# Performance work log

Hardware: AMD Instinct MI355X
Metric: run time of the kernel (lower is better)

Reference implementation:

```python
import jax, jax.numpy as jnp
import numpy as np

B, T, V, D = 128, 128, 64, 32
Q, E, PLM = 5, 8, 768
D_STATIC, N_CLASS = 16, 2
ALPHA = 0.5


def _glorot(key, shape):
    lim = (6.0 / (shape[-2] + shape[-1])) ** 0.5
    return jax.random.uniform(key, shape, jnp.float32, -lim, lim)


def setup_inputs() -> dict:
    key = jax.random.key(0)
    ks = jax.random.split(key, 30)
    data = jax.random.normal(ks[0], (B, T, V), jnp.float32)
    mask = (jax.random.uniform(ks[1], (B, T, V)) < 0.3).astype(jnp.float32)
    P = jnp.concatenate([data, mask], axis=-1)  # [b, t, 2v]
    return {
        "P": P,
        "P_static": jax.random.normal(ks[2], (B, D_STATIC), jnp.float32),
        "P_avg_interval": jax.random.uniform(ks[3], (B, T, V)) * 10.0,
        "P_length": jax.random.randint(ks[4], (B, 1), T // 2, T + 1),
        "P_time": jax.random.uniform(ks[5], (B, T)),
        "P_var_plm_rep_tensor": jax.random.normal(ks[6], (V, PLM), jnp.float32),
        # Value_Encoder: Linear(1, D) + ReLU
        "w_val": _glorot(ks[7], (1, D))[0], "b_val": jnp.zeros((D,), jnp.float32),
        # Time_Encoder: periodic Linear(1, D-1), linear Linear(1, 1)
        "w_per": _glorot(ks[8], (1, D - 1))[0], "b_per": jnp.zeros((D - 1,), jnp.float32),
        "w_lin": _glorot(ks[9], (1, 1))[0], "b_lin": jnp.zeros((1,), jnp.float32),
        "emb1": jax.random.normal(ks[10], (V, D), jnp.float32),
        # prior_to_state MLP: PLM -> 2D -> Q
        "Ws1": _glorot(ks[11], (PLM, 2 * D)), "bs1": jnp.zeros((2 * D,), jnp.float32),
        "Ws2": _glorot(ks[12], (2 * D, Q)), "bs2": jnp.zeros((Q,), jnp.float32),
        # prior_to_graph MLP: PLM -> 2D -> E
        "Wg1": _glorot(ks[13], (PLM, 2 * D)), "bg1": jnp.zeros((2 * D,), jnp.float32),
        "Wg2": _glorot(ks[14], (2 * D, E)), "bg2": jnp.zeros((E,), jnp.float32),
        "rarity_W": jax.random.normal(ks[15], (V, V), jnp.float32),
        # hypernet gate params (nodes_num == Q): W [Q, 2D+1, D], b [Q, D]
        "Wu": _glorot(ks[16], (Q, 2 * D + 1, D)), "bu": _glorot(ks[17], (Q, D)),
        "Wr": _glorot(ks[18], (Q, 2 * D + 1, D)), "br": _glorot(ks[19], (Q, D)),
        "Wcand": _glorot(ks[20], (Q, 2 * D + 1, D)), "bcand": _glorot(ks[21], (Q, D)),
        # static embedding + classifier
        "W_se": _glorot(ks[22], (D_STATIC, V)), "b_se": jnp.zeros((V,), jnp.float32),
        "Wc1": _glorot(ks[23], (2 * V, 200)), "bc1": jnp.zeros((200,), jnp.float32),
        "Wc2": _glorot(ks[24], (200, N_CLASS)), "bc2": jnp.zeros((N_CLASS,), jnp.float32),
    }


def _forward(P, P_static, P_avg_interval, P_length, P_time, P_var_plm_rep_tensor,
             w_val, b_val, w_per, b_per, w_lin, b_lin, emb1,
             Ws1, bs1, Ws2, bs2, Wg1, bg1, Wg2, bg2, rarity_W,
             Wu, bu, Wr, br, Wcand, bcand, W_se, b_se, Wc1, bc1, Wc2, bc2):
    b, t, v2 = P.shape
    v = v2 // 2
    d = emb1.shape[1]
    data, mask = P[:, :, :v], P[:, :, v:]            # [b,t,v] each
    mk = mask[..., None]
    # embeddings: value + absolute time + node embedding, all masked
    value_emb = jax.nn.relu(data[..., None] * w_val + b_val) * mk          # [b,t,v,d]
    tt = P_time[:, :, None, None]                                          # [b,t,1,1]
    time_emb = jnp.concatenate([tt * w_lin + b_lin,
                                jnp.sin(tt * w_per + b_per)], -1) * mk     # [b,t,v,d]
    obs_emb = (value_emb + time_emb + emb1[None, None]) * mk               # [b,t,v,d]

    # PLM-prior hypernet vectors (identical across batch -> computed once, broadcast)
    var_vector = jax.nn.relu(P_var_plm_rep_tensor @ Ws1 + bs1) @ Ws2 + bs2  # [v,Q]
    gvec = jax.nn.relu(P_var_plm_rep_tensor @ Wg1 + bg1) @ Wg2 + bg2        # [v,E]
    gvec = gvec / jnp.maximum(jnp.linalg.norm(gvec, axis=-1, keepdims=True), 1e-12)
    adj = jax.nn.softmax(gvec @ gvec.T, axis=-1)                            # [v,v]

    var_total_obs = mask.sum(axis=1)                                        # [b,v]
    eye = jnp.eye(v, dtype=P.dtype)
    lengths = P_length[:, 0].astype(jnp.int32)                              # [b]

    def gate(inp, W, bb):
        # hypernet-generated per-node GRU gate: einsum('nd,dio->nio') + bmm, fused
        return (jnp.einsum('bvi,vq,qio->bvo', inp, var_vector, W)
                + jnp.einsum('vq,qo->vo', var_vector, bb))

    def step(carry, xs):
        h, out = carry
        cur_obs, m, cur_avg, s = xs
        rarity = ALPHA * jnp.tanh(cur_avg / (var_total_obs + 1.0))          # [b,v]
        rsm = -rarity_W * jnp.abs(rarity[:, :, None] - rarity[:, None, :])  # [b,v,v]
        amask = m[:, :, None] * m[:, None, :]   # rows of unobserved zeroed, observed cols = 1
        cur_adj = adj * (1.0 + rsm) * amask * (1.0 - eye) + eye             # [b,v,v]
        x = jnp.concatenate([cur_obs, rarity[..., None]], -1)               # [b,v,d+1]
        comb = jnp.einsum('bij,bjk->bik', cur_adj, jnp.concatenate([x, h], -1))
        r = jax.nn.sigmoid(gate(comb, Wr, br))
        u = jax.nn.sigmoid(gate(comb, Wu, bu))
        h_r = r * h  # original mutates h[nodes_ind] = r*h[nodes_ind] before candidate
        cand = jnp.tanh(gate(jnp.concatenate([x, h_r], -1), Wcand, bcand))
        h_new = (1.0 - u) * h_r + u * cand
        h = jnp.where((m > 0.5)[..., None], h_new, h)  # scatter only observed nodes
        out = jnp.where((s == lengths - 1)[:, None, None], h, out)
        return (h, out), None

    xs = (jnp.moveaxis(obs_emb, 1, 0), jnp.moveaxis(mask, 1, 0),
          jnp.moveaxis(P_avg_interval, 1, 0), jnp.arange(t, dtype=jnp.int32))
    h0 = jnp.zeros((b, v, d), P.dtype)
    (_, output), _ = jax.lax.scan(step, (h0, jnp.zeros_like(h0)), xs)

    static_emb = P_static @ W_se + b_se                                     # [b,v]
    feat = jnp.concatenate([output.sum(-1), static_emb], -1)                # [b,2v]
    return jax.nn.relu(feat @ Wc1 + bc1) @ Wc2 + bc2                        # [b,n_class]


def reference(P, P_static, P_avg_interval, P_length, P_time, P_var_plm_rep_tensor,
              w_val, b_val, w_per, b_per, w_lin, b_lin, emb1,
              Ws1, bs1, Ws2, bs2, Wg1, bg1, Wg2, bg2, rarity_W,
              Wu, bu, Wr, br, Wcand, bcand, W_se, b_se, Wc1, bc1, Wc2, bc2):
    return _forward(P, P_static, P_avg_interval, P_length, P_time, P_var_plm_rep_tensor,
                    w_val, b_val, w_per, b_per, w_lin, b_lin, emb1,
                    Ws1, bs1, Ws2, bs2, Wg1, bg1, Wg2, bg2, rarity_W,
                    Wu, bu, Wr, br, Wcand, bcand, W_se, b_se, Wc1, bc1, Wc2, bc2)
```

## Files before the change

kernel.cpp:

```cpp
#include <hip/hip_runtime.h>
#include <hip/hip_bf16.h>
#include <math.h>

#define BB 128
#define TT 128
#define VV 64
#define DD 32
#define NQ 5

typedef short bf16x8 __attribute__((ext_vector_type(8)));
typedef float f32x4 __attribute__((ext_vector_type(4)));

#define MFMA(a,b,c) __builtin_amdgcn_mfma_f32_16x16x32_bf16(a,b,c,0,0,0)

__device__ __forceinline__ float sigm(float x){ return 1.0f/(1.0f+__expf(-x)); }
__device__ __forceinline__ float tanhfast(float x){ return 2.0f/(1.0f+__expf(-2.0f*x)) - 1.0f; }
__device__ __forceinline__ unsigned short f2bf(float x){
  unsigned u = __float_as_uint(x);
  u += 0x7FFFu + ((u>>16)&1u);
  return (unsigned short)(u>>16);
}
__device__ __forceinline__ float bf2f(unsigned short h){
  return __uint_as_float(((unsigned)h)<<16);
}

union bfu { bf16x8 v; unsigned u[4]; unsigned short s[8]; };

__device__ __forceinline__ void split8(const float* x, bfu& H, bfu& L){
  #pragma unroll
  for (int i = 0; i < 4; ++i){
    const float a = x[2*i], c = x[2*i+1];
    const __hip_bfloat162 hp = __float22bfloat162_rn(make_float2(a, c));
    unsigned hu; __builtin_memcpy(&hu, &hp, 4);
    H.u[i] = hu;
    const float ah = __uint_as_float(hu << 16);
    const float ch = __uint_as_float(hu & 0xFFFF0000u);
    const __hip_bfloat162 lp = __float22bfloat162_rn(make_float2(a - ah, c - ch));
    unsigned lu; __builtin_memcpy(&lu, &lp, 4);
    L.u[i] = lu;
  }
}

__device__ __forceinline__ void split4(const float* x, unsigned* H, unsigned* L){
  #pragma unroll
  for (int i = 0; i < 2; ++i){
    const float a = x[2*i], c = x[2*i+1];
    const __hip_bfloat162 hp = __float22bfloat162_rn(make_float2(a, c));
    unsigned hu; __builtin_memcpy(&hu, &hp, 4);
    H[i] = hu;
    const float ah = __uint_as_float(hu << 16);
    const float ch = __uint_as_float(hu & 0xFFFF0000u);
    const __hip_bfloat162 lp = __float22bfloat162_rn(make_float2(a - ah, c - ch));
    unsigned lu; __builtin_memcpy(&lu, &lp, 4);
    L[i] = lu;
  }
}


__global__ __launch_bounds__(64)
void k_mlp(const float* __restrict__ Pplm,
           const float* __restrict__ Ws1, const float* __restrict__ bs1,
           const float* __restrict__ Ws2, const float* __restrict__ bs2,
           const float* __restrict__ Wg1, const float* __restrict__ bg1,
           const float* __restrict__ Wg2, const float* __restrict__ bg2,
           float* __restrict__ vv_ws, float* __restrict__ gn_ws)
{
  __shared__ float sH[64], sG[64], sgv[8];
  const int v = blockIdx.x, j = threadIdx.x;
  float a = bs1[j], g = bg1[j];
  for (int k = 0; k < 768; ++k){
    const float p = Pplm[v*768 + k];
    a = fmaf(p, Ws1[k*64 + j], a);
    g = fmaf(p, Wg1[k*64 + j], g);
  }
  sH[j] = fmaxf(a, 0.f);
  sG[j] = fmaxf(g, 0.f);
  __syncthreads();
  if (j < 5){
    float acc = bs2[j];
    for (int k = 0; k < 64; ++k) acc = fmaf(sH[k], Ws2[k*5 + j], acc);
    vv_ws[v*5 + j] = acc;
  }
  if (j < 8){
    float acc = bg2[j];
    for (int k = 0; k < 64; ++k) acc = fmaf(sG[k], Wg2[k*8 + j], acc);
    sgv[j] = acc;
  }
  __syncthreads();
  if (j == 0){
    float n = 0.f;
    for (int e = 0; e < 8; ++e) n += sgv[e]*sgv[e];
    n = fmaxf(sqrtf(n), 1e-12f);
    for (int e = 0; e < 8; ++e) gn_ws[v*8 + e] = sgv[e]/n;
  }
}

__global__ __launch_bounds__(64)
void k_adj(const float* __restrict__ gn_ws, float* __restrict__ adj_ws)
{
  const int v = blockIdx.x, j = threadIdx.x;
  float sc = 0.f;
  #pragma unroll
  for (int e = 0; e < 8; ++e) sc += gn_ws[v*8+e]*gn_ws[j*8+e];
  float mx = sc;
  for (int off = 32; off > 0; off >>= 1) mx = fmaxf(mx, __shfl_xor(mx, off));
  const float ex = __expf(sc - mx);
  float sm = ex;
  for (int off = 32; off > 0; off >>= 1) sm += __shfl_xor(sm, off);
  adj_ws[v*64 + j] = ex / sm;
}

__global__ __launch_bounds__(256)
void k_vto(const float* __restrict__ P, float* __restrict__ vto_ws)
{
  const int idx = blockIdx.x*256 + threadIdx.x;
  if (idx >= BB*VV) return;
  const int b = idx/VV, v = idx%VV;
  float s = 0.f;
  for (int t = 0; t < TT; ++t) s += P[((size_t)(b*TT+t))*128 + 64 + v];
  vto_ws[idx] = s;
}

__global__ __launch_bounds__(256)
void k_bpack(const float* __restrict__ Wr, const float* __restrict__ br,
             const float* __restrict__ Wu, const float* __restrict__ bu,
             const float* __restrict__ Wc, const float* __restrict__ bc,
             unsigned short* __restrict__ Bru, unsigned short* __restrict__ Bcn,
             float* __restrict__ sideRU, float* __restrict__ sideC)
{
  const int idx = blockIdx.x*256 + threadIdx.x;
  if (idx < 20480){
    const int f = idx >> 9, rem = idx & 511, l = rem >> 3, j = rem & 7;
    const int p = f & 1, kt = (f>>1)&1, e = f>>2;
    const int kp = kt*32 + (l>>4)*8 + j;
    const int k = (kp < 32) ? kp : kp + 1;
    const int o = p*16 + (l&15);
    const int q = (e < 5) ? e : e - 5;
    const float* W = (e < 5) ? Wr : Wu;
    Bru[idx] = f2bf(W[(q*65 + k)*32 + o]);
  } else if (idx < 30720){
    const int i2 = idx - 20480;
    const int f = i2 >> 9, rem = i2 & 511, l = rem >> 3, j = rem & 7;
    const int p = f & 1, kt = (f>>1)&1, e = f>>2;
    const int kp = kt*32 + (l>>4)*8 + j;
    const int k = (kp < 32) ? kp : kp + 1;
    const int o = p*16 + (l&15);
    Bcn[i2] = f2bf(Wc[(e*65 + k)*32 + o]);
  } else if (idx < 31360){
    const int i3 = idx - 30720;
    const int e = i3 >> 6, rem = i3 & 63, o = rem >> 1, s = rem & 1;
    const int q = (e < 5) ? e : e - 5;
    float v;
    if (s == 0) v = (e < 5) ? Wr[(q*65 + 32)*32 + o] : Wu[(q*65 + 32)*32 + o];
    else        v = (e < 5) ? br[q*32 + o] : bu[q*32 + o];
    sideRU[i3] = v;
  } else if (idx < 31680){
    const int i4 = idx - 31360;
    const int e = i4 >> 6, rem = i4 & 63, o = rem >> 1, s = rem & 1;
    sideC[i4] = s ? bc[e*32 + o] : Wc[(e*65 + 32)*32 + o];
  }
}


__global__ __launch_bounds__(512, 1)
void tedgn_main(const float* __restrict__ P, const float* __restrict__ Pstatic,
                const float* __restrict__ Pavg, const int* __restrict__ Plen,
                const float* __restrict__ Ptime,
                const float* __restrict__ w_val, const float* __restrict__ b_val,
                const float* __restrict__ w_per, const float* __restrict__ b_per,
                const float* __restrict__ w_lin, const float* __restrict__ b_lin,
                const float* __restrict__ emb1, const float* __restrict__ rarW,
                const float* __restrict__ Wse, const float* __restrict__ bse,
                const float* __restrict__ Wc1, const float* __restrict__ bc1,
                const float* __restrict__ Wc2, const float* __restrict__ bc2,
                const float* __restrict__ vv_ws, const float* __restrict__ adjb_ws,
                const float* __restrict__ vto_ws,
                const unsigned short* __restrict__ Bru_ws,
                const unsigned short* __restrict__ Bc_ws,
                const float* __restrict__ sideRU_ws, const float* __restrict__ sideC_ws,
                float* __restrict__ out)
{
  __shared__ __align__(16) unsigned short B0T[2][2][64][72];
  __shared__ __align__(16) unsigned short s_Wru[20480];
  __shared__ __align__(16) unsigned short s_Wc[10240];
  __shared__ __align__(16) float A1f[4][16][68];
  __shared__ __align__(16) float hrF[4][16][36];
  __shared__ __align__(16) float s_rar[2][64];
  __shared__ __align__(16) float s_m[2][64];
  __shared__ float s_sru[640], s_scd[320];
  __shared__ float s_outf[64][33];
  __shared__ float s_feat[128], s_hid[200];

  const int tid  = threadIdx.x;
  const int lane = tid & 63;
  const int wid  = tid >> 6;
  const int mq   = wid >> 1;
  const int ph   = wid & 1;
  const int l15  = lane & 15;
  const int l16g = lane >> 4;
  const int kgo  = l16g * 8;
  const int R    = mq * 16;
  const int v_own = R + l15;
  const int oo   = ph*16 + l15;
  const int b    = blockIdx.x;
  const int len  = Plen[b];

  for (int i = tid; i < 640; i += 512) s_sru[i] = sideRU_ws[i];
  for (int i = tid; i < 320; i += 512) s_scd[i] = sideC_ws[i];
  {
    const uint4* src1 = (const uint4*)Bru_ws;
    uint4* dst1 = (uint4*)s_Wru;
    for (int i = tid; i < 2560; i += 512) dst1[i] = src1[i];
    const uint4* src2 = (const uint4*)Bc_ws;
    uint4* dst2 = (uint4*)s_Wc;
    for (int i = tid; i < 1280; i += 512) dst2[i] = src2[i];
  }

  float adjb_r[2][8], rarW_r[2][8];
  #pragma unroll
  for (int kt = 0; kt < 2; ++kt)
    #pragma unroll
    for (int j = 0; j < 8; ++j){
      adjb_r[kt][j] = adjb_ws[v_own*64 + kt*32 + kgo + j];
      rarW_r[kt][j] = rarW   [v_own*64 + kt*32 + kgo + j];
    }
  float embr[8], wvr[8], bvr[8], wpr[8], bpr[8];
  #pragma unroll
  for (int j = 0; j < 8; ++j){
    const int d = kgo + j;
    embr[j] = emb1[v_own*DD + d];
    wvr[j]  = w_val[d];
    bvr[j]  = b_val[d];
    wpr[j]  = (d == 0) ? w_lin[0] : w_per[d-1];
    bpr[j]  = (d == 0) ? b_lin[0] : b_per[d-1];
  }
  float vvr[4][NQ];
  #pragma unroll
  for (int j = 0; j < 4; ++j)
    #pragma unroll
    for (int q = 0; q < NQ; ++q)
      vvr[j][q] = vv_ws[(R + l16g*4 + j)*NQ + q];
  const float vto_own = vto_ws[b*VV + v_own];

  float h[4]    = {0.f,0.f,0.f,0.f};
  float outr[4] = {0.f,0.f,0.f,0.f};
  bfu xfH, xfL;
  float rar_own, m_own;

  {
    const float pd = P[(size_t)(b*TT)*128 + v_own];
    const float pm = P[(size_t)(b*TT)*128 + 64 + v_own];
    const float pa = Pavg[(size_t)(b*TT)*VV + v_own];
    const float pt = Ptime[b*TT];
    const float rar_n = 0.5f * tanhfast(pa / (vto_own + 1.f));
    float xv[8];
    #pragma unroll
    for (int j = 0; j < 8; ++j){
      const int d = kgo + j;
      const float tearg = fmaf(pt, wpr[j], bpr[j]);
      const float te = (d == 0) ? tearg : __sinf(tearg);
      const float ve = fmaxf(fmaf(pd, wvr[j], bvr[j]), 0.f);
      xv[j] = (ve + te + embr[j]) * pm;
    }
    split8(xv, xfH, xfL);
    if (ph == 0){
      #pragma unroll
      for (int j = 0; j < 8; ++j){
        B0T[0][0][kgo + j][v_own] = xfH.s[j];
        B0T[0][1][kgo + j][v_own] = xfL.s[j];
      }
      *(uint2*)&B0T[0][0][32 + l15][R + l16g*4] = make_uint2(0u, 0u);
      *(uint2*)&B0T[0][1][32 + l15][R + l16g*4] = make_uint2(0u, 0u);
      if (l16g == 0){
        s_rar[0][v_own] = rar_n;
        s_m[0][v_own]   = pm;
      }
    } else {
      *(uint2*)&B0T[0][0][48 + l15][R + l16g*4] = make_uint2(0u, 0u);
      *(uint2*)&B0T[0][1][48 + l15][R + l16g*4] = make_uint2(0u, 0u);
    }
    rar_own = rar_n;
    m_own   = pm;
  }
  __syncthreads();

  #pragma clang loop unroll(disable)
  for (int t = 0; t < TT; ++t){
    const int cur = t & 1, nxt = cur ^ 1;

    float pd = 0.f, pm = 0.f, pa = 0.f, pt = 0.f;
    const bool more = (t + 1 < TT);
    if (more){
      pd = P[(size_t)(b*TT + t + 1)*128 + v_own];
      pm = P[(size_t)(b*TT + t + 1)*128 + 64 + v_own];
      pa = Pavg[(size_t)(b*TT + t + 1)*VV + v_own];
      pt = Ptime[b*TT + t + 1];
    }

    {
      bfu aAh[2], aAl[2];
      float crar = 0.f;
      #pragma unroll
      for (int kt = 0; kt < 2; ++kt){
        const float4 r0 = *(const float4*)&s_rar[cur][kt*32 + kgo];
        const float4 r1 = *(const float4*)&s_rar[cur][kt*32 + kgo + 4];
        const float4 m0 = *(const float4*)&s_m[cur][kt*32 + kgo];
        const float4 m1 = *(const float4*)&s_m[cur][kt*32 + kgo + 4];
        const float rj[8] = {r0.x,r0.y,r0.z,r0.w,r1.x,r1.y,r1.z,r1.w};
        const float mj[8] = {m0.x,m0.y,m0.z,m0.w,m1.x,m1.y,m1.z,m1.w};
        float av[8];
        #pragma unroll
        for (int j = 0; j < 8; ++j){
          const int k = kt*32 + kgo + j;
          const float e1 = fmaf(-rarW_r[kt][j], fabsf(rar_own - rj[j]), 1.0f);
          const float a  = adjb_r[kt][j] * e1 * (m_own * mj[j]);
          av[j] = (k == v_own) ? 1.0f : a;
          crar = fmaf(av[j], rj[j], crar);
        }
        split8(av, aAh[kt], aAl[kt]);
      }
      crar += __shfl_xor(crar, 16);
      crar += __shfl_xor(crar, 32);
      if (ph == 0 && l16g == 0) A1f[mq][l15][64] = crar;

      #pragma unroll
      for (int ni = 0; ni < 2; ++ni){
        const int n = 2*ph + ni;
        f32x4 acc = {0.f,0.f,0.f,0.f};
        #pragma unroll
        for (int kt = 0; kt < 2; ++kt){
          const bf16x8 bh = *(const bf16x8*)&B0T[cur][0][n*16 + l15][kt*32 + kgo];
          const bf16x8 bl = *(const bf16x8*)&B0T[cur][1][n*16 + l15][kt*32 + kgo];
          acc = MFMA(aAh[kt].v, bh, acc);
          acc = MFMA(aAl[kt].v, bh, acc);
          acc = MFMA(aAh[kt].v, bl, acc);
        }
        const int col = n*16 + l15;
        #pragma unroll
        for (int j = 0; j < 4; ++j) A1f[mq][l16g*4 + j][col] = acc[j];
      }
    }
    __syncthreads();

    float hr[4], uu[4];
    {
      bfu aH[2], aL[2];
      #pragma unroll
      for (int kt = 0; kt < 2; ++kt){
        float xv[8];
        *(float4*)&xv[0] = *(const float4*)&A1f[mq][l15][kt*32 + kgo];
        *(float4*)&xv[4] = *(const float4*)&A1f[mq][l15][kt*32 + kgo + 4];
        split8(xv, aH[kt], aL[kt]);
      }
      float a64f[4];
      #pragma unroll
      for (int j = 0; j < 4; ++j) a64f[j] = A1f[mq][l16g*4 + j][64];

      f32x4 ag[10];
      #pragma unroll
      for (int e = 0; e < 10; ++e){
        const float2 wb = *(const float2*)&s_sru[e*64 + oo*2];
        #pragma unroll
        for (int j = 0; j < 4; ++j) ag[e][j] = fmaf(a64f[j], wb.x, wb.y);
      }
      #pragma unroll
      for (int e = 0; e < 10; ++e){
        const bf16x8 w0 = *(const bf16x8*)&s_Wru[(((e*2+0)*2+ph)*64 + lane)*8];
        const bf16x8 w1 = *(const bf16x8*)&s_Wru[(((e*2+1)*2+ph)*64 + lane)*8];
        ag[e] = MFMA(aH[0].v, w0, ag[e]);
        ag[e] = MFMA(aL[0].v, w0, ag[e]);
        ag[e] = MFMA(aH[1].v, w1, ag[e]);
        ag[e] = MFMA(aL[1].v, w1, ag[e]);
      }
      #pragma unroll
      for (int j = 0; j < 4; ++j){
        const float pr = vvr[j][0]*ag[0][j] + vvr[j][1]*ag[1][j]
                       + vvr[j][2]*ag[2][j] + vvr[j][3]*ag[3][j]
                       + vvr[j][4]*ag[4][j];
        hr[j] = sigm(pr) * h[j];
        hrF[mq][l16g*4 + j][oo] = hr[j];
      }
      #pragma unroll
      for (int j = 0; j < 4; ++j){
        const float pu = vvr[j][0]*ag[5][j] + vvr[j][1]*ag[6][j]
                       + vvr[j][2]*ag[7][j] + vvr[j][3]*ag[8][j]
                       + vvr[j][4]*ag[9][j];
        uu[j] = sigm(pu);
      }
    }
    __syncthreads();

    {
      bfu hH, hL;
      {
        float hv[8];
        *(float4*)&hv[0] = *(const float4*)&hrF[mq][l15][kgo];
        *(float4*)&hv[4] = *(const float4*)&hrF[mq][l15][kgo + 4];
        split8(hv, hH, hL);
      }
      float rar_cj[4], m_cj[4];
      #pragma unroll
      for (int j = 0; j < 4; ++j){
        rar_cj[j] = s_rar[cur][R + l16g*4 + j];
        m_cj[j]   = s_m[cur][R + l16g*4 + j];
      }
      f32x4 ag[5];
      #pragma unroll
      for (int e = 0; e < 5; ++e){
        const float2 wb = *(const float2*)&s_scd[e*64 + oo*2];
        #pragma unroll
        for (int j = 0; j < 4; ++j) ag[e][j] = fmaf(rar_cj[j], wb.x, wb.y);
      }
      #pragma unroll
      for (int e = 0; e < 5; ++e){
        const bf16x8 w0 = *(const bf16x8*)&s_Wc[(((e*2+0)*2+ph)*64 + lane)*8];
        const bf16x8 w1 = *(const bf16x8*)&s_Wc[(((e*2+1)*2+ph)*64 + lane)*8];
        ag[e] = MFMA(xfH.v, w0, ag[e]);
        ag[e] = MFMA(xfL.v, w0, ag[e]);
        ag[e] = MFMA(hH.v,  w1, ag[e]);
        ag[e] = MFMA(hL.v,  w1, ag[e]);
      }
      const bool snap = (t == len - 1);
      #pragma unroll
      for (int j = 0; j < 4; ++j){
        const float pc = vvr[j][0]*ag[0][j] + vvr[j][1]*ag[1][j]
                       + vvr[j][2]*ag[2][j] + vvr[j][3]*ag[3][j]
                       + vvr[j][4]*ag[4][j];
        const float cd = tanhfast(pc);
        const float hn = fmaf(uu[j], cd - hr[j], hr[j]);
        const float hf = (m_cj[j] > 0.5f) ? hn : h[j];
        h[j] = hf;
        if (snap) outr[j] = hf;
      }
      {
        unsigned H2[2], L2[2];
        split4(h, H2, L2);
        *(uint2*)&B0T[nxt][0][32 + oo][R + l16g*4] = make_uint2(H2[0], H2[1]);
        *(uint2*)&B0T[nxt][1][32 + oo][R + l16g*4] = make_uint2(L2[0], L2[1]);
      }
      if (more){
        const float rar_n = 0.5f * tanhfast(pa / (vto_own + 1.f));
        float xv[8];
        #pragma unroll
        for (int j = 0; j < 8; ++j){
          const int d = kgo + j;
          const float tearg = fmaf(pt, wpr[j], bpr[j]);
          const float te = (d == 0) ? tearg : __sinf(tearg);
          const float ve = fmaxf(fmaf(pd, wvr[j], bvr[j]), 0.f);
          xv[j] = (ve + te + embr[j]) * pm;
        }
        split8(xv, xfH, xfL);
        if (ph == 0){
          #pragma unroll
          for (int j = 0; j < 8; ++j){
            B0T[nxt][0][kgo + j][v_own] = xfH.s[j];
            B0T[nxt][1][kgo + j][v_own] = xfL.s[j];
          }
          if (l16g == 0){
            s_rar[nxt][v_own] = rar_n;
            s_m[nxt][v_own]   = pm;
          }
        }
        rar_own = rar_n;
        m_own   = pm;
      }
    }
    __syncthreads();
  }

  #pragma unroll
  for (int j = 0; j < 4; ++j)
    s_outf[R + l16g*4 + j][oo] = outr[j];
  __syncthreads();
  if (tid < VV){
    float s = 0.f;
    #pragma unroll
    for (int d = 0; d < DD; ++d) s += s_outf[tid][d];
    s_feat[tid] = s;
  } else if (tid < 2*VV){
    const int v = tid - VV;
    float se = bse[v];
    #pragma unroll
    for (int k = 0; k < 16; ++k) se = fmaf(Pstatic[b*16 + k], Wse[k*VV + v], se);
    s_feat[VV + v] = se;
  }
  __syncthreads();
  if (tid < 200){
    float a = bc1[tid];
    for (int k = 0; k < 128; ++k) a = fmaf(s_feat[k], Wc1[k*200 + tid], a);
    s_hid[tid] = fmaxf(a, 0.f);
  }
  __syncthreads();
  if (tid < 2){
    float a = bc2[tid];
    for (int k = 0; k < 200; ++k) a = fmaf(s_hid[k], Wc2[k*2 + tid], a);
    out[b*2 + tid] = a;
  }
}


extern "C" void kernel_launch(void* const* d_in, const int* in_sizes, int n_in,
                              void* d_out, int out_size, void* d_ws, size_t ws_size,
                              hipStream_t stream) {
  (void)in_sizes; (void)n_in; (void)out_size; (void)ws_size;
  const float* P       = (const float*)d_in[0];
  const float* Pstatic = (const float*)d_in[1];
  const float* Pavg    = (const float*)d_in[2];
  const int*   Plen    = (const int*)  d_in[3];
  const float* Ptime   = (const float*)d_in[4];
  const float* Pplm    = (const float*)d_in[5];
  const float* w_val   = (const float*)d_in[6];
  const float* b_val   = (const float*)d_in[7];
  const float* w_per   = (const float*)d_in[8];
  const float* b_per   = (const float*)d_in[9];
  const float* w_lin   = (const float*)d_in[10];
  const float* b_lin   = (const float*)d_in[11];
  const float* emb1    = (const float*)d_in[12];
  const float* Ws1     = (const float*)d_in[13];
  const float* bs1     = (const float*)d_in[14];
  const float* Ws2     = (const float*)d_in[15];
  const float* bs2     = (const float*)d_in[16];
  const float* Wg1     = (const float*)d_in[17];
  const float* bg1     = (const float*)d_in[18];
  const float* Wg2     = (const float*)d_in[19];
  const float* bg2     = (const float*)d_in[20];
  const float* rarW    = (const float*)d_in[21];
  const float* Wu      = (const float*)d_in[22];
  const float* bu      = (const float*)d_in[23];
  const float* Wr      = (const float*)d_in[24];
  const float* br      = (const float*)d_in[25];
  const float* Wcand   = (const float*)d_in[26];
  const float* bcand   = (const float*)d_in[27];
  const float* Wse     = (const float*)d_in[28];
  const float* bse     = (const float*)d_in[29];
  const float* Wc1     = (const float*)d_in[30];
  const float* bc1     = (const float*)d_in[31];
  const float* Wc2     = (const float*)d_in[32];
  const float* bc2     = (const float*)d_in[33];

  float* ws = (float*)d_ws;
  float*          vv_ws   = ws;
  float*          gn_ws   = ws + 320;
  float*          adjb_ws = ws + 832;
  float*          vto_ws  = ws + 4928;
  unsigned short* Bru_ws  = (unsigned short*)(ws + 13120);
  unsigned short* Bc_ws   = (unsigned short*)(ws + 23360);
  float*          sideRU_ws = ws + 28480;
  float*          sideC_ws  = ws + 29120;

  k_mlp  <<<64, 64, 0, stream>>>(Pplm, Ws1, bs1, Ws2, bs2, Wg1, bg1, Wg2, bg2, vv_ws, gn_ws);
  k_adj  <<<64, 64, 0, stream>>>(gn_ws, adjb_ws);
  k_vto  <<<(BB*VV + 255)/256, 256, 0, stream>>>(P, vto_ws);
  k_bpack<<<124, 256, 0, stream>>>(Wr, br, Wu, bu, Wcand, bcand, Bru_ws, Bc_ws, sideRU_ws, sideC_ws);

  tedgn_main<<<BB, 512, 0, stream>>>(P, Pstatic, Pavg, Plen, Ptime,
                                     w_val, b_val, w_per, b_per, w_lin, b_lin,
                                     emb1, rarW, Wse, bse, Wc1, bc1, Wc2, bc2,
                                     vv_ws, adjb_ws, vto_ws,
                                     Bru_ws, Bc_ws, sideRU_ws, sideC_ws,
                                     (float*)d_out);
}
```

Measured before the change: 586.2 us.

## Transpose MFMA operand roles to drop A1f staging and one barrier per step

Swaps the A/B operand roles in the graph-aggregation and gate MFMAs, so each lane ends up holding the rows its own node needs. The aggregated features then feed the gate MFMAs straight from registers instead of going through the A1f shared buffer and an extra __syncthreads each timestep. The packed weight layouts in k_bpack are permuted to match the new fragment order. The next-step input embedding is computed earlier to overlap with the MFMAs, and per-node state becomes scalars instead of 4-row arrays. In exchange, the h writeback now uses scalar scattered shared stores, which may add bank conflicts.

Measured after the change: 639.3 us. 9.1% more time.

```diff
diff --git a/kernel.cpp b/kernel.cpp
--- a/kernel.cpp
+++ b/kernel.cpp
@@ -38,21 +38,6 @@
     const __hip_bfloat162 lp = __float22bfloat162_rn(make_float2(a - ah, c - ch));
     unsigned lu; __builtin_memcpy(&lu, &lp, 4);
     L.u[i] = lu;
-  }
-}
-
-__device__ __forceinline__ void split4(const float* x, unsigned* H, unsigned* L){
-  #pragma unroll
-  for (int i = 0; i < 2; ++i){
-    const float a = x[2*i], c = x[2*i+1];
-    const __hip_bfloat162 hp = __float22bfloat162_rn(make_float2(a, c));
-    unsigned hu; __builtin_memcpy(&hu, &hp, 4);
-    H[i] = hu;
-    const float ah = __uint_as_float(hu << 16);
-    const float ch = __uint_as_float(hu & 0xFFFF0000u);
-    const __hip_bfloat162 lp = __float22bfloat162_rn(make_float2(a - ah, c - ch));
-    unsigned lu; __builtin_memcpy(&lu, &lp, 4);
-    L[i] = lu;
   }
 }
 
@@ -131,20 +116,21 @@
   const int idx = blockIdx.x*256 + threadIdx.x;
   if (idx < 20480){
     const int f = idx >> 9, rem = idx & 511, l = rem >> 3, j = rem & 7;
-    const int p = f & 1, kt = (f>>1)&1, e = f>>2;
-    const int kp = kt*32 + (l>>4)*8 + j;
-    const int k = (kp < 32) ? kp : kp + 1;
-    const int o = p*16 + (l&15);
+    const int ph = f & 1, kt = (f>>1)&1, e = f>>2;
+    const int l15 = l & 15, l16g = l >> 4;
+    const int fslot = (kt*2 + (j>>2))*16 + l16g*4 + (j&3);
+    const int k = (fslot < 32) ? fslot : fslot + 1;
+    const int o = ph*16 + l15;
     const int q = (e < 5) ? e : e - 5;
     const float* W = (e < 5) ? Wr : Wu;
     Bru[idx] = f2bf(W[(q*65 + k)*32 + o]);
   } else if (idx < 30720){
     const int i2 = idx - 20480;
     const int f = i2 >> 9, rem = i2 & 511, l = rem >> 3, j = rem & 7;
-    const int p = f & 1, kt = (f>>1)&1, e = f>>2;
-    const int kp = kt*32 + (l>>4)*8 + j;
-    const int k = (kp < 32) ? kp : kp + 1;
-    const int o = p*16 + (l&15);
+    const int ph = f & 1, kt = (f>>1)&1, e = f>>2;
+    const int l15 = l & 15, l16g = l >> 4;
+    const int k = (kt == 0) ? (l16g*8 + j) : (33 + l16g*8 + j);
+    const int o = ph*16 + l15;
     Bcn[i2] = f2bf(Wc[(e*65 + k)*32 + o]);
   } else if (idx < 31360){
     const int i3 = idx - 30720;
@@ -183,7 +169,6 @@
   __shared__ __align__(16) unsigned short B0T[2][2][64][72];
   __shared__ __align__(16) unsigned short s_Wru[20480];
   __shared__ __align__(16) unsigned short s_Wc[10240];
-  __shared__ __align__(16) float A1f[4][16][68];
   __shared__ __align__(16) float hrF[4][16][36];
   __shared__ __align__(16) float s_rar[2][64];
   __shared__ __align__(16) float s_m[2][64];
@@ -201,7 +186,7 @@
   const int kgo  = l16g * 8;
   const int R    = mq * 16;
   const int v_own = R + l15;
-  const int oo   = ph*16 + l15;
+  const int ob   = ph*16 + l16g*4;
   const int b    = blockIdx.x;
   const int len  = Plen[b];
 
@@ -234,17 +219,14 @@
     wpr[j]  = (d == 0) ? w_lin[0] : w_per[d-1];
     bpr[j]  = (d == 0) ? b_lin[0] : b_per[d-1];
   }
-  float vvr[4][NQ];
+  float vv_own[NQ];
   #pragma unroll
-  for (int j = 0; j < 4; ++j)
-    #pragma unroll
-    for (int q = 0; q < NQ; ++q)
-      vvr[j][q] = vv_ws[(R + l16g*4 + j)*NQ + q];
+  for (int q = 0; q < NQ; ++q) vv_own[q] = vv_ws[v_own*NQ + q];
   const float vto_own = vto_ws[b*VV + v_own];
 
   float h[4]    = {0.f,0.f,0.f,0.f};
   float outr[4] = {0.f,0.f,0.f,0.f};
-  bfu xfH, xfL;
+  bfu xfH, xfL, xfnH, xfnL;
   float rar_own, m_own;
 
   {
@@ -287,6 +269,7 @@
   #pragma clang loop unroll(disable)
   for (int t = 0; t < TT; ++t){
     const int cur = t & 1, nxt = cur ^ 1;
+    const float rar_cur = rar_own, m_cur = m_own;
 
     float pd = 0.f, pm = 0.f, pa = 0.f, pt = 0.f;
     const bool more = (t + 1 < TT);
@@ -297,95 +280,118 @@
       pt = Ptime[b*TT + t + 1];
     }
 
-    {
-      bfu aAh[2], aAl[2];
-      float crar = 0.f;
+    bfu aAh[2], aAl[2];
+    float crar = 0.f;
+    #pragma unroll
+    for (int kt = 0; kt < 2; ++kt){
+      const float4 r0 = *(const float4*)&s_rar[cur][kt*32 + kgo];
+      const float4 r1 = *(const float4*)&s_rar[cur][kt*32 + kgo + 4];
+      const float4 m0 = *(const float4*)&s_m[cur][kt*32 + kgo];
+      const float4 m1 = *(const float4*)&s_m[cur][kt*32 + kgo + 4];
+      const float rj[8] = {r0.x,r0.y,r0.z,r0.w,r1.x,r1.y,r1.z,r1.w};
+      const float mj[8] = {m0.x,m0.y,m0.z,m0.w,m1.x,m1.y,m1.z,m1.w};
+      float av[8];
+      #pragma unroll
+      for (int j = 0; j < 8; ++j){
+        const int k = kt*32 + kgo + j;
+        const float e1 = fmaf(-rarW_r[kt][j], fabsf(rar_cur - rj[j]), 1.0f);
+        const float a  = adjb_r[kt][j] * e1 * (m_cur * mj[j]);
+        av[j] = (k == v_own) ? 1.0f : a;
+        crar = fmaf(av[j], rj[j], crar);
+      }
+      split8(av, aAh[kt], aAl[kt]);
+    }
+    crar += __shfl_xor(crar, 16);
+    crar += __shfl_xor(crar, 32);
+
+    f32x4 Dv[4];
+    #pragma unroll
+    for (int ft = 0; ft < 4; ++ft){
+      f32x4 acc = {0.f,0.f,0.f,0.f};
       #pragma unroll
       for (int kt = 0; kt < 2; ++kt){
-        const float4 r0 = *(const float4*)&s_rar[cur][kt*32 + kgo];
-        const float4 r1 = *(const float4*)&s_rar[cur][kt*32 + kgo + 4];
-        const float4 m0 = *(const float4*)&s_m[cur][kt*32 + kgo];
-        const float4 m1 = *(const float4*)&s_m[cur][kt*32 + kgo + 4];
-        const float rj[8] = {r0.x,r0.y,r0.z,r0.w,r1.x,r1.y,r1.z,r1.w};
-        const float mj[8] = {m0.x,m0.y,m0.z,m0.w,m1.x,m1.y,m1.z,m1.w};
-        float av[8];
+        const bf16x8 ah = *(const bf16x8*)&B0T[cur][0][ft*16 + l15][kt*32 + kgo];
+        const bf16x8 al = *(const bf16x8*)&B0T[cur][1][ft*16 + l15][kt*32 + kgo];
+        acc = MFMA(ah, aAh[kt].v, acc);
+        acc = MFMA(al, aAh[kt].v, acc);
+        acc = MFMA(ah, aAl[kt].v, acc);
+      }
+      Dv[ft] = acc;
+    }
+
+    if (more){
+      const float rar_n = 0.5f * tanhfast(pa / (vto_own + 1.f));
+      float xv[8];
+      #pragma unroll
+      for (int j = 0; j < 8; ++j){
+        const int d = kgo + j;
+        const float tearg = fmaf(pt, wpr[j], bpr[j]);
+        const float te = (d == 0) ? tearg : __sinf(tearg);
+        const float ve = fmaxf(fmaf(pd, wvr[j], bvr[j]), 0.f);
+        xv[j] = (ve + te + embr[j]) * pm;
+      }
+      split8(xv, xfnH, xfnL);
+      if (ph == 0){
         #pragma unroll
         for (int j = 0; j < 8; ++j){
-          const int k = kt*32 + kgo + j;
-          const float e1 = fmaf(-rarW_r[kt][j], fabsf(rar_own - rj[j]), 1.0f);
-          const float a  = adjb_r[kt][j] * e1 * (m_own * mj[j]);
-          av[j] = (k == v_own) ? 1.0f : a;
-          crar = fmaf(av[j], rj[j], crar);
+          B0T[nxt][0][kgo + j][v_own] = xfnH.s[j];
+          B0T[nxt][1][kgo + j][v_own] = xfnL.s[j];
         }
-        split8(av, aAh[kt], aAl[kt]);
-      }
-      crar += __shfl_xor(crar, 16);
-      crar += __shfl_xor(crar, 32);
-      if (ph == 0 && l16g == 0) A1f[mq][l15][64] = crar;
-
-      #pragma unroll
-      for (int ni = 0; ni < 2; ++ni){
-        const int n = 2*ph + ni;
-        f32x4 acc = {0.f,0.f,0.f,0.f};
+        if (l16g == 0){
+          s_rar[nxt][v_own] = rar_n;
+          s_m[nxt][v_own]   = pm;
+        }
+      }
+      rar_own = rar_n;
+      m_own   = pm;
+    }
+
+    bfu cfH[2], cfL[2];
+    #pragma unroll
+    for (int kt = 0; kt < 2; ++kt){
+      float f8[8];
+      #pragma unroll
+      for (int j = 0; j < 8; ++j) f8[j] = Dv[kt*2 + (j>>2)][j&3];
+      split8(f8, cfH[kt], cfL[kt]);
+    }
+
+    float hr[4], uu[4];
+    {
+      f32x4 ag[10];
+      #pragma unroll
+      for (int e = 0; e < 10; ++e){
+        const float4 sp0 = *(const float4*)&s_sru[e*64 + ob*2];
+        const float4 sp1 = *(const float4*)&s_sru[e*64 + ob*2 + 4];
+        ag[e][0] = fmaf(crar, sp0.x, sp0.y);
+        ag[e][1] = fmaf(crar, sp0.z, sp0.w);
+        ag[e][2] = fmaf(crar, sp1.x, sp1.y);
+        ag[e][3] = fmaf(crar, sp1.z, sp1.w);
+      }
+      #pragma unroll
+      for (int e = 0; e < 10; ++e){
         #pragma unroll
         for (int kt = 0; kt < 2; ++kt){
-          const bf16x8 bh = *(const bf16x8*)&B0T[cur][0][n*16 + l15][kt*32 + kgo];
-          const bf16x8 bl = *(const bf16x8*)&B0T[cur][1][n*16 + l15][kt*32 + kgo];
-          acc = MFMA(aAh[kt].v, bh, acc);
-          acc = MFMA(aAl[kt].v, bh, acc);
-          acc = MFMA(aAh[kt].v, bl, acc);
+          const bf16x8 w = *(const bf16x8*)&s_Wru[(((e*2+kt)*2+ph)*64 + lane)*8];
+          ag[e] = MFMA(w, cfH[kt].v, ag[e]);
+          ag[e] = MFMA(w, cfL[kt].v, ag[e]);
         }
-        const int col = n*16 + l15;
-        #pragma unroll
-        for (int j = 0; j < 4; ++j) A1f[mq][l16g*4 + j][col] = acc[j];
-      }
-    }
-    __syncthreads();
-
-    float hr[4], uu[4];
-    {
-      bfu aH[2], aL[2];
-      #pragma unroll
-      for (int kt = 0; kt < 2; ++kt){
-        float xv[8];
-        *(float4*)&xv[0] = *(const float4*)&A1f[mq][l15][kt*32 + kgo];
-        *(float4*)&xv[4] = *(const float4*)&A1f[mq][l15][kt*32 + kgo + 4];
-        split8(xv, aH[kt], aL[kt]);
-      }
-      float a64f[4];
-      #pragma unroll
-      for (int j = 0; j < 4; ++j) a64f[j] = A1f[mq][l16g*4 + j][64];
-
-      f32x4 ag[10];
-      #pragma unroll
-      for (int e = 0; e < 10; ++e){
-        const float2 wb = *(const float2*)&s_sru[e*64 + oo*2];
-        #pragma unroll
-        for (int j = 0; j < 4; ++j) ag[e][j] = fmaf(a64f[j], wb.x, wb.y);
-      }
-      #pragma unroll
-      for (int e = 0; e < 10; ++e){
-        const bf16x8 w0 = *(const bf16x8*)&s_Wru[(((e*2+0)*2+ph)*64 + lane)*8];
-        const bf16x8 w1 = *(const bf16x8*)&s_Wru[(((e*2+1)*2+ph)*64 + lane)*8];
-        ag[e] = MFMA(aH[0].v, w0, ag[e]);
-        ag[e] = MFMA(aL[0].v, w0, ag[e]);
-        ag[e] = MFMA(aH[1].v, w1, ag[e]);
-        ag[e] = MFMA(aL[1].v, w1, ag[e]);
-      }
-      #pragma unroll
-      for (int j = 0; j < 4; ++j){
-        const float pr = vvr[j][0]*ag[0][j] + vvr[j][1]*ag[1][j]
-                       + vvr[j][2]*ag[2][j] + vvr[j][3]*ag[3][j]
-                       + vvr[j][4]*ag[4][j];
-        hr[j] = sigm(pr) * h[j];
-        hrF[mq][l16g*4 + j][oo] = hr[j];
-      }
-      #pragma unroll
-      for (int j = 0; j < 4; ++j){
-        const float pu = vvr[j][0]*ag[5][j] + vvr[j][1]*ag[6][j]
-                       + vvr[j][2]*ag[7][j] + vvr[j][3]*ag[8][j]
-                       + vvr[j][4]*ag[9][j];
-        uu[j] = sigm(pu);
+      }
+      float hr4[4];
+      #pragma unroll
+      for (int jj = 0; jj < 4; ++jj){
+        const float pr = vv_own[0]*ag[0][jj] + vv_own[1]*ag[1][jj]
+                       + vv_own[2]*ag[2][jj] + vv_own[3]*ag[3][jj]
+                       + vv_own[4]*ag[4][jj];
+        hr[jj] = sigm(pr) * h[jj];
+        hr4[jj] = hr[jj];
+      }
+      *(float4*)&hrF[mq][l15][ob] = make_float4(hr4[0], hr4[1], hr4[2], hr4[3]);
+      #pragma unroll
+      for (int jj = 0; jj < 4; ++jj){
+        const float pu = vv_own[0]*ag[5][jj] + vv_own[1]*ag[6][jj]
+                       + vv_own[2]*ag[7][jj] + vv_own[3]*ag[8][jj]
+                       + vv_own[4]*ag[9][jj];
+        uu[jj] = sigm(pu);
       }
     }
     __syncthreads();
@@ -398,79 +404,51 @@
         *(float4*)&hv[4] = *(const float4*)&hrF[mq][l15][kgo + 4];
         split8(hv, hH, hL);
       }
-      float rar_cj[4], m_cj[4];
-      #pragma unroll
-      for (int j = 0; j < 4; ++j){
-        rar_cj[j] = s_rar[cur][R + l16g*4 + j];
-        m_cj[j]   = s_m[cur][R + l16g*4 + j];
-      }
       f32x4 ag[5];
       #pragma unroll
       for (int e = 0; e < 5; ++e){
-        const float2 wb = *(const float2*)&s_scd[e*64 + oo*2];
-        #pragma unroll
-        for (int j = 0; j < 4; ++j) ag[e][j] = fmaf(rar_cj[j], wb.x, wb.y);
+        const float4 sp0 = *(const float4*)&s_scd[e*64 + ob*2];
+        const float4 sp1 = *(const float4*)&s_scd[e*64 + ob*2 + 4];
+        ag[e][0] = fmaf(rar_cur, sp0.x, sp0.y);
+        ag[e][1] = fmaf(rar_cur, sp0.z, sp0.w);
+        ag[e][2] = fmaf(rar_cur, sp1.x, sp1.y);
+        ag[e][3] = fmaf(rar_cur, sp1.z, sp1.w);
       }
       #pragma unroll
       for (int e = 0; e < 5; ++e){
         const bf16x8 w0 = *(const bf16x8*)&s_Wc[(((e*2+0)*2+ph)*64 + lane)*8];
         const bf16x8 w1 = *(const bf16x8*)&s_Wc[(((e*2+1)*2+ph)*64 + lane)*8];
-        ag[e] = MFMA(xfH.v, w0, ag[e]);
-        ag[e] = MFMA(xfL.v, w0, ag[e]);
-        ag[e] = MFMA(hH.v,  w1, ag[e]);
-        ag[e] = MFMA(hL.v,  w1, ag[e]);
+        ag[e] = MFMA(w0, xfH.v, ag[e]);
+        ag[e] = MFMA(w0, xfL.v, ag[e]);
+        ag[e] = MFMA(w1, hH.v,  ag[e]);
+        ag[e] = MFMA(w1, hL.v,  ag[e]);
       }
       const bool snap = (t == len - 1);
       #pragma unroll
-      for (int j = 0; j < 4; ++j){
-        const float pc = vvr[j][0]*ag[0][j] + vvr[j][1]*ag[1][j]
-                       + vvr[j][2]*ag[2][j] + vvr[j][3]*ag[3][j]
-                       + vvr[j][4]*ag[4][j];
+      for (int jj = 0; jj < 4; ++jj){
+        const float pc = vv_own[0]*ag[0][jj] + vv_own[1]*ag[1][jj]
+                       + vv_own[2]*ag[2][jj] + vv_own[3]*ag[3][jj]
+                       + vv_own[4]*ag[4][jj];
         const float cd = tanhfast(pc);
-        const float hn = fmaf(uu[j], cd - hr[j], hr[j]);
-        const float hf = (m_cj[j] > 0.5f) ? hn : h[j];
-        h[j] = hf;
-        if (snap) outr[j] = hf;
-      }
-      {
-        unsigned H2[2], L2[2];
-        split4(h, H2, L2);
-        *(uint2*)&B0T[nxt][0][32 + oo][R + l16g*4] = make_uint2(H2[0], H2[1]);
-        *(uint2*)&B0T[nxt][1][32 + oo][R + l16g*4] = make_uint2(L2[0], L2[1]);
-      }
-      if (more){
-        const float rar_n = 0.5f * tanhfast(pa / (vto_own + 1.f));
-        float xv[8];
-        #pragma unroll
-        for (int j = 0; j < 8; ++j){
-          const int d = kgo + j;
-          const float tearg = fmaf(pt, wpr[j], bpr[j]);
-          const float te = (d == 0) ? tearg : __sinf(tearg);
-          const float ve = fmaxf(fmaf(pd, wvr[j], bvr[j]), 0.f);
-          xv[j] = (ve + te + embr[j]) * pm;
-        }
-        split8(xv, xfH, xfL);
-        if (ph == 0){
-          #pragma unroll
-          for (int j = 0; j < 8; ++j){
-            B0T[nxt][0][kgo + j][v_own] = xfH.s[j];
-            B0T[nxt][1][kgo + j][v_own] = xfL.s[j];
-          }
-          if (l16g == 0){
-            s_rar[nxt][v_own] = rar_n;
-            s_m[nxt][v_own]   = pm;
-          }
-        }
-        rar_own = rar_n;
-        m_own   = pm;
-      }
+        const float hn = fmaf(uu[jj], cd - hr[jj], hr[jj]);
+        const float hf = (m_cur > 0.5f) ? hn : h[jj];
+        h[jj] = hf;
+        if (snap) outr[jj] = hf;
+      }
+      #pragma unroll
+      for (int jj = 0; jj < 4; ++jj){
+        const unsigned short hh = f2bf(h[jj]);
+        B0T[nxt][0][32 + ob + jj][v_own] = hh;
+        B0T[nxt][1][32 + ob + jj][v_own] = f2bf(h[jj] - bf2f(hh));
+      }
+      if (more){ xfH = xfnH; xfL = xfnL; }
     }
     __syncthreads();
   }
 
   #pragma unroll
-  for (int j = 0; j < 4; ++j)
-    s_outf[R + l16g*4 + j][oo] = outr[j];
+  for (int jj = 0; jj < 4; ++jj)
+    s_outf[v_own][ob + jj] = outr[jj];
   __syncthreads();
   if (tid < VV){
     float s = 0.f;
```
